# Kernel optimization log

Hardware: AMD Instinct MI355X
Metric: run time of the kernel (lower is better)

Reference implementation:

```python
import jax, jax.numpy as jnp
import numpy as np

DIM_IN, HID, N = 3, 512, 65536


def _xavier(key, shape):
    fan_in, fan_out = shape[1], shape[0]
    lim = np.sqrt(6.0 / (fan_in + fan_out))
    return jax.random.uniform(key, shape, jnp.float32, -lim, lim)


def setup_inputs() -> dict:
    key = jax.random.key(0)
    names_shapes = [
        ("W1", (HID, DIM_IN)), ("b1", (HID, 1)),
        ("Uz1", (HID, DIM_IN)), ("Wz1", (HID, HID)), ("bz1", (HID, 1)),
        ("Ug1", (HID, DIM_IN)), ("Wg1", (HID, HID)), ("bg1", (HID, 1)),
        ("Ur1", (HID, DIM_IN)), ("Wr1", (HID, HID)), ("br1", (HID, 1)),
        ("Uh1", (HID, DIM_IN)), ("Wh1", (HID, HID)), ("bh1", (HID, 1)),
        ("Uz2", (HID, DIM_IN)), ("Wz2", (HID, HID)), ("bz2", (HID, 1)),
        ("Ug2", (HID, DIM_IN)), ("Wg2", (HID, HID)), ("bg2", (HID, 1)),
        ("Ur2", (HID, DIM_IN)), ("Wr2", (HID, HID)), ("br2", (HID, 1)),
        ("Uh2", (HID, DIM_IN)), ("Wh2", (HID, HID)), ("bh2", (HID, 1)),
        ("W", (1, HID)), ("b", (1, 1)),
    ]
    keys = jax.random.split(key, len(names_shapes) + 1)
    inp = {"x": jax.random.normal(keys[0], (DIM_IN, N), jnp.float32)}
    for k, (nm, sh) in zip(keys[1:], names_shapes):
        inp[nm] = _xavier(k, sh)
    return inp


def reference(x, W1, b1, Uz1, Wz1, bz1, Ug1, Wg1, bg1, Ur1, Wr1, br1,
              Uh1, Wh1, bh1, Uz2, Wz2, bz2, Ug2, Wg2, bg2, Ur2, Wr2, br2,
              Uh2, Wh2, bh2, W, b):
    # x: (dim_in, N); all hidden states are (hidden_sz, N)
    S1 = jnp.tanh(W1 @ x + b1)
    Z1 = jnp.tanh(Uz1 @ x + Wz1 @ S1 + bz1)
    G1 = jnp.tanh(Ug1 @ x + Wg1 @ S1 + bg1)
    R1 = jnp.tanh(Ur1 @ x + Wr1 @ S1 + br1)
    H1 = jnp.tanh(Uh1 @ x + Wh1 @ (S1 * R1) + bh1)
    S2 = (1.0 - G1) * H1 + Z1 * S1
    Z2 = jnp.tanh(Uz2 @ x + Wz2 @ S2 + bz2)
    G2 = jnp.tanh(Ug2 @ x + Wg2 @ S2 + bg2)
    R2 = jnp.tanh(Ur2 @ x + Wr2 @ S2 + br2)
    H2 = jnp.tanh(Uh2 @ x + Wh2 @ (S2 * R2) + bh2)
    S3 = (1.0 - G2) * H2 + Z2 * S2
    return W @ S3 + b  # (1, N)
```

## Files before the change

### kernel.cpp

```cpp
#include <hip/hip_runtime.h>

typedef unsigned short u16;
typedef unsigned int   u32;
typedef short bf16x8 __attribute__((ext_vector_type(8)));
typedef float f32x4  __attribute__((ext_vector_type(4)));
typedef unsigned short u16x4 __attribute__((ext_vector_type(4)));
typedef unsigned int   u32x2 __attribute__((ext_vector_type(2)));

#define HID   512
#define NT    64
#define NCOL  65536
#define KTILES 17
#define BBUF  (KTILES * 4 * 512)
#define WMAT_ELEMS (KTILES * 32 * 512)

__device__ __forceinline__ float bf2f(u16 v) {
  union { u32 u; float f; } t; t.u = ((u32)v) << 16; return t.f;
}
__device__ __forceinline__ u16 f2bf(float f) {
  union { float f; u32 u; } t; t.f = f;
  u32 r = t.u + 0x7fffu + ((t.u >> 16) & 1u);
  return (u16)(r >> 16);
}
__device__ __forceinline__ float lo16(u32 v) { return bf2f((u16)(v & 0xffffu)); }
__device__ __forceinline__ float hi16(u32 v) { return bf2f((u16)(v >> 16)); }
__device__ __forceinline__ u32 pk2(float lo, float hi) {
  u32 r;
  asm("v_cvt_pk_bf16_f32 %0, %1, %2" : "=v"(r) : "v"(lo), "v"(hi));
  return r;
}
__device__ __forceinline__ float ldv(const void* p, int i, int isbf) {
  return isbf ? bf2f(((const u16*)p)[i]) : ((const float*)p)[i];
}
__device__ __forceinline__ float tanh_fast(float x) {
  float e = __builtin_amdgcn_exp2f(x * 2.8853900817779268f);
  return 1.0f - 2.0f * __builtin_amdgcn_rcpf(e + 1.0f);
}

__device__ __forceinline__ int boff(int c, int k) {
  return ((k >> 5) * 4 + (c >> 4)) * 512 + ((k >> 3) & 3) * 128 + (c & 15) * 8 + (k & 7);
}

__global__ void sniff_kernel(const u16* x, u32* flag) {
  if (threadIdx.x == 0 && blockIdx.x == 0) {
    int cnt = 0;
    for (int i = 0; i < 256; i++) {
      u32 e = (x[i] >> 7) & 0xFFu;
      if (e == 0u || (e >= 100u && e <= 140u)) cnt++;
    }
    *flag = (cnt >= 220) ? 1u : 0u;
  }
}

struct PrepArgs {
  const void* U[9]; const void* B[9];
  const void* Wout; const void* bout;
  float* dst; const u32* flag;
};

__global__ void prep_kernel(PrepArgs a) {
  int t = blockIdx.x * 256 + threadIdx.x;
  const int isbf = (int)*a.flag;
  if (t < 9 * 512) {
    int m = t >> 9, r = t & 511;
    float4 v;
    v.x = ldv(a.U[m], r * 3 + 0, isbf);
    v.y = ldv(a.U[m], r * 3 + 1, isbf);
    v.z = ldv(a.U[m], r * 3 + 2, isbf);
    v.w = ldv(a.B[m], r, isbf);
    ((float4*)a.dst)[t] = v;
  } else if (t < 9 * 512 + 512) {
    int r = t - 9 * 512;
    a.dst[9 * 2048 + r] = ldv(a.Wout, r, isbf);
    if (r == 0) a.dst[9 * 2048 + 512] = ldv(a.bout, 0, isbf);
  }
}

struct SwzArgs {
  const void* src[8];
  const void* usrc[8];
  const void* bsrc[8];
  u16* dst; const u32* flag;
};

__global__ void swizzle_kernel(SwzArgs a) {
  const int isbf = (int)*a.flag;
  int t = blockIdx.x * 256 + threadIdx.x;
  int m    = t / (KTILES * 32 * 64);
  int rem  = t - m * (KTILES * 32 * 64);
  int tile = rem >> 6;
  int lane = rem & 63;
  int kb = tile >> 5, rt = tile & 31;
  int row = rt * 16 + (lane & 15);
  int kk  = (lane >> 4) * 8;
  u16 tmp[8];
  if (kb < 16) {
    int k = kb * 32 + kk;
    if (isbf) {
      const u16* s = (const u16*)a.src[m] + row * 512 + k;
#pragma unroll
      for (int j = 0; j < 8; j++) tmp[j] = s[j];
    } else {
      const float* s = (const float*)a.src[m] + row * 512 + k;
#pragma unroll
      for (int j = 0; j < 8; j++) tmp[j] = f2bf(s[j]);
    }
  } else {
#pragma unroll
    for (int j = 0; j < 8; j++) {
      int kidx = kk + j;
      float v = (kidx < 3) ? ldv(a.usrc[m], row * 3 + kidx, isbf)
              : (kidx == 3) ? ldv(a.bsrc[m], row, isbf)
              : 0.0f;
      tmp[j] = f2bf(v);
    }
  }
  uint4* d = (uint4*)(a.dst + (size_t)m * WMAT_ELEMS + (size_t)tile * 512 + lane * 8);
  *d = *(const uint4*)tmp;
}

struct KArgs {
  const void* x;
  const u16* ws;
  const float4* ub;
  const u32* flag;
  void* out;
};

__device__ __forceinline__ void gemm64(f32x4 acc[4][4],
    const u16* __restrict__ wmat, const u16* ldsB, int rowslab, int lane)
{
  const u16* abase = wmat + (size_t)(rowslab * 4) * 512 + lane * 8;
  const u16* bbase = ldsB + lane * 8;
  bf16x8 a[3][4];
#pragma unroll
  for (int p = 0; p < 2; p++)
#pragma unroll
    for (int i = 0; i < 4; i++)
      a[p][i] = *(const bf16x8*)(abase + (size_t)p * 16384 + i * 512);
#pragma unroll
  for (int kb = 0; kb < KTILES; kb++) {
    if (kb + 2 < KTILES) {
#pragma unroll
      for (int i = 0; i < 4; i++)
        a[(kb + 2) % 3][i] = *(const bf16x8*)(abase + (size_t)(kb + 2) * 16384 + i * 512);
    }
    bf16x8 b[4];
#pragma unroll
    for (int ct = 0; ct < 4; ct++)
      b[ct] = *(const bf16x8*)(bbase + (kb * 4 + ct) * 512);
    __builtin_amdgcn_s_setprio(1);
#pragma unroll
    for (int rt = 0; rt < 4; rt++)
#pragma unroll
      for (int ct = 0; ct < 4; ct++)
        acc[rt][ct] = __builtin_amdgcn_mfma_f32_16x16x32_bf16(a[kb % 3][rt], b[ct], acc[rt][ct], 0, 0, 0);
    __builtin_amdgcn_s_setprio(0);
  }
}

__global__ __launch_bounds__(512, 2) void pdenet_kernel(KArgs ka) {
  __shared__ __align__(16) u16 ldsS[BBUF];
  __shared__ __align__(16) u16 ldsR[BBUF];
  __shared__ float xs[3 * NT];

  const int isbf = (int)*ka.flag;
  const int tid  = threadIdx.x;
  const int rowslab = tid >> 6;
  const int lane = tid & 63;
  const int l15  = lane & 15;
  const int quad = lane >> 4;
  const int c0   = blockIdx.x * NT;

  if (tid < 3 * NT)
    xs[tid] = ldv(ka.x, (tid >> 6) * NCOL + c0 + (tid & 63), isbf);
  __syncthreads();

  {
    int r = tid;
    float4 w = ka.ub[8 * 512 + r];
#pragma unroll 4
    for (int cc = 0; cc < NT; cc++) {
      int c = (cc + lane) & 63;
      float s = tanh_fast(w.x * xs[c] + w.y * xs[NT + c] + w.z * xs[2 * NT + c] + w.w);
      ldsS[boff(c, r)] = f2bf(s);
    }
  }

  {
#pragma unroll
    for (int rep = 0; rep < 4; rep++) {
      int e = tid + rep * 512;
      int c = e >> 5, j = e & 31;
      float v = (j == 0) ? xs[c] : (j == 1) ? xs[NT + c]
              : (j == 2) ? xs[2 * NT + c] : (j == 3) ? 1.0f : 0.0f;
      u16 bv = f2bf(v);
      int o = boff(c, 512 + j);
      ldsS[o] = bv;
      ldsR[o] = bv;
    }
  }
  __syncthreads();

  u32 zpk[4][4][2], opk[4][4][2];

#pragma unroll
  for (int layer = 0; layer < 2; layer++) {
    const int g0 = layer * 4;

    {
      f32x4 acc[4][4] = {};
      gemm64(acc, ka.ws + (size_t)(g0 + 0) * WMAT_ELEMS, ldsS, rowslab, lane);
#pragma unroll
      for (int rt = 0; rt < 4; rt++)
#pragma unroll
        for (int ct = 0; ct < 4; ct++) {
          zpk[rt][ct][0] = pk2(tanh_fast(acc[rt][ct][0]), tanh_fast(acc[rt][ct][1]));
          zpk[rt][ct][1] = pk2(tanh_fast(acc[rt][ct][2]), tanh_fast(acc[rt][ct][3]));
        }
    }
    {
      f32x4 acc[4][4] = {};
      gemm64(acc, ka.ws + (size_t)(g0 + 1) * WMAT_ELEMS, ldsS, rowslab, lane);
#pragma unroll
      for (int rt = 0; rt < 4; rt++)
#pragma unroll
        for (int ct = 0; ct < 4; ct++) {
          opk[rt][ct][0] = pk2(1.0f - tanh_fast(acc[rt][ct][0]),
                               1.0f - tanh_fast(acc[rt][ct][1]));
          opk[rt][ct][1] = pk2(1.0f - tanh_fast(acc[rt][ct][2]),
                               1.0f - tanh_fast(acc[rt][ct][3]));
        }
    }
    {
      f32x4 acc[4][4] = {};
      gemm64(acc, ka.ws + (size_t)(g0 + 2) * WMAT_ELEMS, ldsS, rowslab, lane);
#pragma unroll
      for (int rt = 0; rt < 4; rt++)
#pragma unroll
        for (int ct = 0; ct < 4; ct++) {
          int c  = ct * 16 + l15;
          int rb = rowslab * 64 + rt * 16 + quad * 4;
          int o  = boff(c, rb);
          u16x4 sv4 = *(const u16x4*)&ldsS[o];
          float sv0 = bf2f(sv4[0]), sv1 = bf2f(sv4[1]);
          float sv2 = bf2f(sv4[2]), sv3 = bf2f(sv4[3]);
          u32x2 sr;
          sr[0] = pk2(sv0 * tanh_fast(acc[rt][ct][0]), sv1 * tanh_fast(acc[rt][ct][1]));
          sr[1] = pk2(sv2 * tanh_fast(acc[rt][ct][2]), sv3 * tanh_fast(acc[rt][ct][3]));
          u32 zp0 = zpk[rt][ct][0], zp1 = zpk[rt][ct][1];
          zpk[rt][ct][0] = pk2(lo16(zp0) * sv0, hi16(zp0) * sv1);
          zpk[rt][ct][1] = pk2(lo16(zp1) * sv2, hi16(zp1) * sv3);
          *(u32x2*)&ldsR[o] = sr;
        }
    }
    __syncthreads();
    {
      f32x4 acc[4][4] = {};
      gemm64(acc, ka.ws + (size_t)(g0 + 3) * WMAT_ELEMS, ldsR, rowslab, lane);
#pragma unroll
      for (int rt = 0; rt < 4; rt++)
#pragma unroll
        for (int ct = 0; ct < 4; ct++) {
          int c  = ct * 16 + l15;
          int rb = rowslab * 64 + rt * 16 + quad * 4;
          u32 zp0 = zpk[rt][ct][0], zp1 = zpk[rt][ct][1];
          u32 op0 = opk[rt][ct][0], op1 = opk[rt][ct][1];
          u32x2 sn;
          sn[0] = pk2(lo16(op0) * tanh_fast(acc[rt][ct][0]) + lo16(zp0),
                      hi16(op0) * tanh_fast(acc[rt][ct][1]) + hi16(zp0));
          sn[1] = pk2(lo16(op1) * tanh_fast(acc[rt][ct][2]) + lo16(zp1),
                      hi16(op1) * tanh_fast(acc[rt][ct][3]) + hi16(zp1));
          *(u32x2*)&ldsS[boff(c, rb)] = sn;
        }
    }
    __syncthreads();
  }

  {
    int c   = tid >> 3;
    int seg = tid & 7;
    const float* wv = (const float*)(ka.ub + 9 * 512);
    const float4* w4 = (const float4*)(wv + seg * 64);
    float p = 0.0f;
#pragma unroll
    for (int j = 0; j < 16; j++) {
      u16x4 sv = *(const u16x4*)&ldsS[boff(c, seg * 64 + j * 4)];
      float4 w = w4[j];
      p += w.x * bf2f(sv[0]) + w.y * bf2f(sv[1]) + w.z * bf2f(sv[2]) + w.w * bf2f(sv[3]);
    }
    p += __shfl_xor(p, 1);
    p += __shfl_xor(p, 2);
    p += __shfl_xor(p, 4);
    if (seg == 0) {
      float res = p + wv[512];
      if (isbf) ((u16*)ka.out)[c0 + c] = f2bf(res);
      else      ((float*)ka.out)[c0 + c] = res;
    }
  }
}

extern "C" void kernel_launch(void* const* d_in, const int* in_sizes, int n_in,
                              void* d_out, int out_size, void* d_ws, size_t ws_size,
                              hipStream_t stream) {
  static const int widx[8] = {4, 7, 10, 13, 16, 19, 22, 25};
  static const int uidx[8] = {3, 6, 9, 12, 15, 18, 21, 24};
  static const int bidx[8] = {5, 8, 11, 14, 17, 20, 23, 26};

  u16*   ws16  = (u16*)d_ws;
  u32*   flagp = (u32*)((char*)d_ws + (size_t)8 * WMAT_ELEMS * 2);
  float* ubp   = (float*)((char*)d_ws + (size_t)8 * WMAT_ELEMS * 2 + 16);

  hipLaunchKernelGGL(sniff_kernel, dim3(1), dim3(64), 0, stream,
                     (const u16*)d_in[0], flagp);

  PrepArgs pa;
  for (int i = 0; i < 8; i++) { pa.U[i] = d_in[uidx[i]]; pa.B[i] = d_in[bidx[i]]; }
  pa.U[8] = d_in[1]; pa.B[8] = d_in[2];
  pa.Wout = d_in[27]; pa.bout = d_in[28];
  pa.dst = ubp; pa.flag = flagp;
  hipLaunchKernelGGL(prep_kernel, dim3(20), dim3(256), 0, stream, pa);

  SwzArgs sa;
  for (int i = 0; i < 8; i++) {
    sa.src[i]  = d_in[widx[i]];
    sa.usrc[i] = d_in[uidx[i]];
    sa.bsrc[i] = d_in[bidx[i]];
  }
  sa.dst  = ws16;
  sa.flag = flagp;
  hipLaunchKernelGGL(swizzle_kernel, dim3(1088), dim3(256), 0, stream, sa);

  KArgs ka;
  ka.x    = d_in[0];
  ka.ws   = ws16;
  ka.ub   = (const float4*)ubp;
  ka.flag = flagp;
  ka.out  = d_out;
  hipLaunchKernelGGL(pdenet_kernel, dim3(NCOL / NT), dim3(512), 0, stream, ka);
}
```

Measured before the change: 421.1 us.

## Overlap previous gate's tanh epilogue with next gate's MFMA loop

Adds a pipelined GEMM variant that, inside each K-tile iteration, applies tanh to one 16x16 accumulator tile of the previous gate (Z or G) and packs it to bf16 while the current gate's MFMAs issue. sched_group_barrier hints interleave the MFMAs with VALU work. The A-operand prefetch buffer also drops from three stages to two, which frees registers for the extra live accumulator set. The aim is to hide the transcendental epilogue behind matrix work, at the cost of keeping two 4x4 accumulator arrays live and possibly more register pressure or spills under launch_bounds(512,2).

```diff
diff --git a/kernel.cpp b/kernel.cpp
--- a/kernel.cpp
+++ b/kernel.cpp
@@ -132,18 +132,16 @@
 {
   const u16* abase = wmat + (size_t)(rowslab * 4) * 512 + lane * 8;
   const u16* bbase = ldsB + lane * 8;
-  bf16x8 a[3][4];
-#pragma unroll
-  for (int p = 0; p < 2; p++)
-#pragma unroll
-    for (int i = 0; i < 4; i++)
-      a[p][i] = *(const bf16x8*)(abase + (size_t)p * 16384 + i * 512);
+  bf16x8 a[2][4];
+#pragma unroll
+  for (int i = 0; i < 4; i++)
+    a[0][i] = *(const bf16x8*)(abase + i * 512);
 #pragma unroll
   for (int kb = 0; kb < KTILES; kb++) {
-    if (kb + 2 < KTILES) {
+    if (kb + 1 < KTILES) {
 #pragma unroll
       for (int i = 0; i < 4; i++)
-        a[(kb + 2) % 3][i] = *(const bf16x8*)(abase + (size_t)(kb + 2) * 16384 + i * 512);
+        a[(kb + 1) & 1][i] = *(const bf16x8*)(abase + (size_t)(kb + 1) * 16384 + i * 512);
     }
     bf16x8 b[4];
 #pragma unroll
@@ -154,8 +152,52 @@
     for (int rt = 0; rt < 4; rt++)
 #pragma unroll
       for (int ct = 0; ct < 4; ct++)
-        acc[rt][ct] = __builtin_amdgcn_mfma_f32_16x16x32_bf16(a[kb % 3][rt], b[ct], acc[rt][ct], 0, 0, 0);
+        acc[rt][ct] = __builtin_amdgcn_mfma_f32_16x16x32_bf16(a[kb & 1][rt], b[ct], acc[rt][ct], 0, 0, 0);
     __builtin_amdgcn_s_setprio(0);
+  }
+}
+
+template<int MODE>
+__device__ __forceinline__ void gemm64_pipe(f32x4 acc[4][4],
+    const u16* __restrict__ wmat, const u16* ldsB, int rowslab, int lane,
+    f32x4 accP[4][4], u32 dstP[4][4][2])
+{
+  const u16* abase = wmat + (size_t)(rowslab * 4) * 512 + lane * 8;
+  const u16* bbase = ldsB + lane * 8;
+  bf16x8 a[2][4];
+#pragma unroll
+  for (int i = 0; i < 4; i++)
+    a[0][i] = *(const bf16x8*)(abase + i * 512);
+#pragma unroll
+  for (int kb = 0; kb < KTILES; kb++) {
+    if (kb + 1 < KTILES) {
+#pragma unroll
+      for (int i = 0; i < 4; i++)
+        a[(kb + 1) & 1][i] = *(const bf16x8*)(abase + (size_t)(kb + 1) * 16384 + i * 512);
+    }
+    bf16x8 b[4];
+#pragma unroll
+    for (int ct = 0; ct < 4; ct++)
+      b[ct] = *(const bf16x8*)(bbase + (kb * 4 + ct) * 512);
+#pragma unroll
+    for (int rt = 0; rt < 4; rt++)
+#pragma unroll
+      for (int ct = 0; ct < 4; ct++)
+        acc[rt][ct] = __builtin_amdgcn_mfma_f32_16x16x32_bf16(a[kb & 1][rt], b[ct], acc[rt][ct], 0, 0, 0);
+    if (kb >= 1) {
+      const int i  = kb - 1;
+      const int rt = i >> 2;
+      const int ct = i & 3;
+      float t0 = tanh_fast(accP[rt][ct][0]);
+      float t1 = tanh_fast(accP[rt][ct][1]);
+      float t2 = tanh_fast(accP[rt][ct][2]);
+      float t3 = tanh_fast(accP[rt][ct][3]);
+      if (MODE) { t0 = 1.0f - t0; t1 = 1.0f - t1; t2 = 1.0f - t2; t3 = 1.0f - t3; }
+      dstP[rt][ct][0] = pk2(t0, t1);
+      dstP[rt][ct][1] = pk2(t2, t3);
+    }
+    __builtin_amdgcn_sched_group_barrier(0x008, 16, 0);
+    __builtin_amdgcn_sched_group_barrier(0x002, 30, 0);
   }
 }
 
@@ -208,33 +250,17 @@
   for (int layer = 0; layer < 2; layer++) {
     const int g0 = layer * 4;
 
+    f32x4 accZ[4][4] = {};
+    gemm64(accZ, ka.ws + (size_t)(g0 + 0) * WMAT_ELEMS, ldsS, rowslab, lane);
+
+    f32x4 accG[4][4] = {};
+    gemm64_pipe<0>(accG, ka.ws + (size_t)(g0 + 1) * WMAT_ELEMS, ldsS, rowslab,
+                   lane, accZ, zpk);
+
     {
       f32x4 acc[4][4] = {};
-      gemm64(acc, ka.ws + (size_t)(g0 + 0) * WMAT_ELEMS, ldsS, rowslab, lane);
-#pragma unroll
-      for (int rt = 0; rt < 4; rt++)
-#pragma unroll
-        for (int ct = 0; ct < 4; ct++) {
-          zpk[rt][ct][0] = pk2(tanh_fast(acc[rt][ct][0]), tanh_fast(acc[rt][ct][1]));
-          zpk[rt][ct][1] = pk2(tanh_fast(acc[rt][ct][2]), tanh_fast(acc[rt][ct][3]));
-        }
-    }
-    {
-      f32x4 acc[4][4] = {};
-      gemm64(acc, ka.ws + (size_t)(g0 + 1) * WMAT_ELEMS, ldsS, rowslab, lane);
-#pragma unroll
-      for (int rt = 0; rt < 4; rt++)
-#pragma unroll
-        for (int ct = 0; ct < 4; ct++) {
-          opk[rt][ct][0] = pk2(1.0f - tanh_fast(acc[rt][ct][0]),
-                               1.0f - tanh_fast(acc[rt][ct][1]));
-          opk[rt][ct][1] = pk2(1.0f - tanh_fast(acc[rt][ct][2]),
-                               1.0f - tanh_fast(acc[rt][ct][3]));
-        }
-    }
-    {
-      f32x4 acc[4][4] = {};
-      gemm64(acc, ka.ws + (size_t)(g0 + 2) * WMAT_ELEMS, ldsS, rowslab, lane);
+      gemm64_pipe<1>(acc, ka.ws + (size_t)(g0 + 2) * WMAT_ELEMS, ldsS, rowslab,
+                     lane, accG, opk);
 #pragma unroll
       for (int rt = 0; rt < 4; rt++)
 #pragma unroll
```

Measured after the change: 424.7 us. No clear change (+0.9%).

## Split row slabs across 16 waves with 1024-thread blocks

Applied to the files above, without the earlier changes.

Doubles the block to 1024 threads so each wave computes a 32-row slab (2 row tiles) instead of 64 rows, cutting per-wave accumulator and A-fragment registers and lowering the A prefetch depth from 2 tiles to 1. The S1 init, bias-row fill and final dot-product reduction are re-split across the larger thread count. The goal is more waves in flight to hide global weight-load latency, at the cost of each wave re-reading the shared B tiles from LDS for half as many MFMAs, a shallower prefetch, and more barrier participants.

```diff
diff --git a/kernel.cpp b/kernel.cpp
--- a/kernel.cpp
+++ b/kernel.cpp
@@ -127,23 +127,21 @@
   void* out;
 };
 
-__device__ __forceinline__ void gemm64(f32x4 acc[4][4],
-    const u16* __restrict__ wmat, const u16* ldsB, int rowslab, int lane)
+__device__ __forceinline__ void gemm64(f32x4 acc[2][4],
+    const u16* __restrict__ wmat, const u16* ldsB, int wave, int lane)
 {
-  const u16* abase = wmat + (size_t)(rowslab * 4) * 512 + lane * 8;
+  const u16* abase = wmat + (size_t)(wave * 2) * 512 + lane * 8;
   const u16* bbase = ldsB + lane * 8;
-  bf16x8 a[3][4];
-#pragma unroll
-  for (int p = 0; p < 2; p++)
-#pragma unroll
-    for (int i = 0; i < 4; i++)
-      a[p][i] = *(const bf16x8*)(abase + (size_t)p * 16384 + i * 512);
+  bf16x8 a[2][2];
+#pragma unroll
+  for (int i = 0; i < 2; i++)
+    a[0][i] = *(const bf16x8*)(abase + i * 512);
 #pragma unroll
   for (int kb = 0; kb < KTILES; kb++) {
-    if (kb + 2 < KTILES) {
-#pragma unroll
-      for (int i = 0; i < 4; i++)
-        a[(kb + 2) % 3][i] = *(const bf16x8*)(abase + (size_t)(kb + 2) * 16384 + i * 512);
+    if (kb + 1 < KTILES) {
+#pragma unroll
+      for (int i = 0; i < 2; i++)
+        a[(kb + 1) & 1][i] = *(const bf16x8*)(abase + (size_t)(kb + 1) * 16384 + i * 512);
     }
     bf16x8 b[4];
 #pragma unroll
@@ -151,22 +149,22 @@
       b[ct] = *(const bf16x8*)(bbase + (kb * 4 + ct) * 512);
     __builtin_amdgcn_s_setprio(1);
 #pragma unroll
-    for (int rt = 0; rt < 4; rt++)
+    for (int rt = 0; rt < 2; rt++)
 #pragma unroll
       for (int ct = 0; ct < 4; ct++)
-        acc[rt][ct] = __builtin_amdgcn_mfma_f32_16x16x32_bf16(a[kb % 3][rt], b[ct], acc[rt][ct], 0, 0, 0);
+        acc[rt][ct] = __builtin_amdgcn_mfma_f32_16x16x32_bf16(a[kb & 1][rt], b[ct], acc[rt][ct], 0, 0, 0);
     __builtin_amdgcn_s_setprio(0);
   }
 }
 
-__global__ __launch_bounds__(512, 2) void pdenet_kernel(KArgs ka) {
+__global__ __launch_bounds__(1024, 4) void pdenet_kernel(KArgs ka) {
   __shared__ __align__(16) u16 ldsS[BBUF];
   __shared__ __align__(16) u16 ldsR[BBUF];
   __shared__ float xs[3 * NT];
 
   const int isbf = (int)*ka.flag;
   const int tid  = threadIdx.x;
-  const int rowslab = tid >> 6;
+  const int wave = tid >> 6;
   const int lane = tid & 63;
   const int l15  = lane & 15;
   const int quad = lane >> 4;
@@ -177,11 +175,12 @@
   __syncthreads();
 
   {
-    int r = tid;
+    int r  = tid & 511;
+    int ch = tid >> 9;
     float4 w = ka.ub[8 * 512 + r];
 #pragma unroll 4
-    for (int cc = 0; cc < NT; cc++) {
-      int c = (cc + lane) & 63;
+    for (int cc = 0; cc < 32; cc++) {
+      int c = ch * 32 + ((cc + lane) & 31);
       float s = tanh_fast(w.x * xs[c] + w.y * xs[NT + c] + w.z * xs[2 * NT + c] + w.w);
       ldsS[boff(c, r)] = f2bf(s);
     }
@@ -189,8 +188,8 @@
 
   {
 #pragma unroll
-    for (int rep = 0; rep < 4; rep++) {
-      int e = tid + rep * 512;
+    for (int rep = 0; rep < 2; rep++) {
+      int e = tid + rep * 1024;
       int c = e >> 5, j = e & 31;
       float v = (j == 0) ? xs[c] : (j == 1) ? xs[NT + c]
               : (j == 2) ? xs[2 * NT + c] : (j == 3) ? 1.0f : 0.0f;
@@ -202,17 +201,17 @@
   }
   __syncthreads();
 
-  u32 zpk[4][4][2], opk[4][4][2];
+  u32 zpk[2][4][2], opk[2][4][2];
 
 #pragma unroll
   for (int layer = 0; layer < 2; layer++) {
     const int g0 = layer * 4;
 
     {
-      f32x4 acc[4][4] = {};
-      gemm64(acc, ka.ws + (size_t)(g0 + 0) * WMAT_ELEMS, ldsS, rowslab, lane);
-#pragma unroll
-      for (int rt = 0; rt < 4; rt++)
+      f32x4 acc[2][4] = {};
+      gemm64(acc, ka.ws + (size_t)(g0 + 0) * WMAT_ELEMS, ldsS, wave, lane);
+#pragma unroll
+      for (int rt = 0; rt < 2; rt++)
 #pragma unroll
         for (int ct = 0; ct < 4; ct++) {
           zpk[rt][ct][0] = pk2(tanh_fast(acc[rt][ct][0]), tanh_fast(acc[rt][ct][1]));
@@ -220,10 +219,10 @@
         }
     }
     {
-      f32x4 acc[4][4] = {};
-      gemm64(acc, ka.ws + (size_t)(g0 + 1) * WMAT_ELEMS, ldsS, rowslab, lane);
-#pragma unroll
-      for (int rt = 0; rt < 4; rt++)
+      f32x4 acc[2][4] = {};
+      gemm64(acc, ka.ws + (size_t)(g0 + 1) * WMAT_ELEMS, ldsS, wave, lane);
+#pragma unroll
+      for (int rt = 0; rt < 2; rt++)
 #pragma unroll
         for (int ct = 0; ct < 4; ct++) {
           opk[rt][ct][0] = pk2(1.0f - tanh_fast(acc[rt][ct][0]),
@@ -233,14 +232,14 @@
         }
     }
     {
-      f32x4 acc[4][4] = {};
-      gemm64(acc, ka.ws + (size_t)(g0 + 2) * WMAT_ELEMS, ldsS, rowslab, lane);
-#pragma unroll
-      for (int rt = 0; rt < 4; rt++)
+      f32x4 acc[2][4] = {};
+      gemm64(acc, ka.ws + (size_t)(g0 + 2) * WMAT_ELEMS, ldsS, wave, lane);
+#pragma unroll
+      for (int rt = 0; rt < 2; rt++)
 #pragma unroll
         for (int ct = 0; ct < 4; ct++) {
           int c  = ct * 16 + l15;
-          int rb = rowslab * 64 + rt * 16 + quad * 4;
+          int rb = wave * 32 + rt * 16 + quad * 4;
           int o  = boff(c, rb);
           u16x4 sv4 = *(const u16x4*)&ldsS[o];
           float sv0 = bf2f(sv4[0]), sv1 = bf2f(sv4[1]);
@@ -256,14 +255,14 @@
     }
     __syncthreads();
     {
-      f32x4 acc[4][4] = {};
-      gemm64(acc, ka.ws + (size_t)(g0 + 3) * WMAT_ELEMS, ldsR, rowslab, lane);
-#pragma unroll
-      for (int rt = 0; rt < 4; rt++)
+      f32x4 acc[2][4] = {};
+      gemm64(acc, ka.ws + (size_t)(g0 + 3) * WMAT_ELEMS, ldsR, wave, lane);
+#pragma unroll
+      for (int rt = 0; rt < 2; rt++)
 #pragma unroll
         for (int ct = 0; ct < 4; ct++) {
           int c  = ct * 16 + l15;
-          int rb = rowslab * 64 + rt * 16 + quad * 4;
+          int rb = wave * 32 + rt * 16 + quad * 4;
           u32 zp0 = zpk[rt][ct][0], zp1 = zpk[rt][ct][1];
           u32 op0 = opk[rt][ct][0], op1 = opk[rt][ct][1];
           u32x2 sn;
@@ -278,20 +277,21 @@
   }
 
   {
-    int c   = tid >> 3;
-    int seg = tid & 7;
+    int c   = tid >> 4;
+    int seg = tid & 15;
     const float* wv = (const float*)(ka.ub + 9 * 512);
-    const float4* w4 = (const float4*)(wv + seg * 64);
+    const float4* w4 = (const float4*)(wv + seg * 32);
     float p = 0.0f;
 #pragma unroll
-    for (int j = 0; j < 16; j++) {
-      u16x4 sv = *(const u16x4*)&ldsS[boff(c, seg * 64 + j * 4)];
+    for (int j = 0; j < 8; j++) {
+      u16x4 sv = *(const u16x4*)&ldsS[boff(c, seg * 32 + j * 4)];
       float4 w = w4[j];
       p += w.x * bf2f(sv[0]) + w.y * bf2f(sv[1]) + w.z * bf2f(sv[2]) + w.w * bf2f(sv[3]);
     }
     p += __shfl_xor(p, 1);
     p += __shfl_xor(p, 2);
     p += __shfl_xor(p, 4);
+    p += __shfl_xor(p, 8);
     if (seg == 0) {
       float res = p + wv[512];
       if (isbf) ((u16*)ka.out)[c0 + c] = f2bf(res);
@@ -337,5 +337,5 @@
   ka.ub   = (const float4*)ubp;
   ka.flag = flagp;
   ka.out  = d_out;
-  hipLaunchKernelGGL(pdenet_kernel, dim3(NCOL / NT), dim3(512), 0, stream, ka);
-}
+  hipLaunchKernelGGL(pdenet_kernel, dim3(NCOL / NT), dim3(1024), 0, stream, ka);
+}
```

Result: slower. 465.6 us (+10.6%).

## Spill 1-G gate to LDS and shrink A-prefetch to double buffer to cut VGPRs

Applied to the files above, without the earlier changes.

Moves the G-gate GEMM after the R-gate GEMM and stores (1-G) in the S buffer in LDS, after a barrier, instead of keeping it packed in registers. The last GEMM's epilogue then reads it back from LDS. The A-operand prefetch also goes from triple to double buffering. Both changes lower register pressure so the 512-thread, 2-block launch bound spills less, at the cost of extra LDS traffic and a shorter global-load prefetch distance.

```diff
diff --git a/kernel.cpp b/kernel.cpp
--- a/kernel.cpp
+++ b/kernel.cpp
@@ -132,18 +132,16 @@
 {
   const u16* abase = wmat + (size_t)(rowslab * 4) * 512 + lane * 8;
   const u16* bbase = ldsB + lane * 8;
-  bf16x8 a[3][4];
-#pragma unroll
-  for (int p = 0; p < 2; p++)
-#pragma unroll
-    for (int i = 0; i < 4; i++)
-      a[p][i] = *(const bf16x8*)(abase + (size_t)p * 16384 + i * 512);
+  bf16x8 a[2][4];
+#pragma unroll
+  for (int i = 0; i < 4; i++)
+    a[0][i] = *(const bf16x8*)(abase + i * 512);
 #pragma unroll
   for (int kb = 0; kb < KTILES; kb++) {
-    if (kb + 2 < KTILES) {
+    if (kb + 1 < KTILES) {
 #pragma unroll
       for (int i = 0; i < 4; i++)
-        a[(kb + 2) % 3][i] = *(const bf16x8*)(abase + (size_t)(kb + 2) * 16384 + i * 512);
+        a[(kb + 1) & 1][i] = *(const bf16x8*)(abase + (size_t)(kb + 1) * 16384 + i * 512);
     }
     bf16x8 b[4];
 #pragma unroll
@@ -154,7 +152,7 @@
     for (int rt = 0; rt < 4; rt++)
 #pragma unroll
       for (int ct = 0; ct < 4; ct++)
-        acc[rt][ct] = __builtin_amdgcn_mfma_f32_16x16x32_bf16(a[kb % 3][rt], b[ct], acc[rt][ct], 0, 0, 0);
+        acc[rt][ct] = __builtin_amdgcn_mfma_f32_16x16x32_bf16(a[kb & 1][rt], b[ct], acc[rt][ct], 0, 0, 0);
     __builtin_amdgcn_s_setprio(0);
   }
 }
@@ -202,7 +200,7 @@
   }
   __syncthreads();
 
-  u32 zpk[4][4][2], opk[4][4][2];
+  u32 zpk[4][4][2];
 
 #pragma unroll
   for (int layer = 0; layer < 2; layer++) {
@@ -217,19 +215,6 @@
         for (int ct = 0; ct < 4; ct++) {
           zpk[rt][ct][0] = pk2(tanh_fast(acc[rt][ct][0]), tanh_fast(acc[rt][ct][1]));
           zpk[rt][ct][1] = pk2(tanh_fast(acc[rt][ct][2]), tanh_fast(acc[rt][ct][3]));
-        }
-    }
-    {
-      f32x4 acc[4][4] = {};
-      gemm64(acc, ka.ws + (size_t)(g0 + 1) * WMAT_ELEMS, ldsS, rowslab, lane);
-#pragma unroll
-      for (int rt = 0; rt < 4; rt++)
-#pragma unroll
-        for (int ct = 0; ct < 4; ct++) {
-          opk[rt][ct][0] = pk2(1.0f - tanh_fast(acc[rt][ct][0]),
-                               1.0f - tanh_fast(acc[rt][ct][1]));
-          opk[rt][ct][1] = pk2(1.0f - tanh_fast(acc[rt][ct][2]),
-                               1.0f - tanh_fast(acc[rt][ct][3]));
         }
     }
     {
@@ -254,7 +239,22 @@
           *(u32x2*)&ldsR[o] = sr;
         }
     }
-    __syncthreads();
+    {
+      f32x4 acc[4][4] = {};
+      gemm64(acc, ka.ws + (size_t)(g0 + 1) * WMAT_ELEMS, ldsS, rowslab, lane);
+      __syncthreads();
+#pragma unroll
+      for (int rt = 0; rt < 4; rt++)
+#pragma unroll
+        for (int ct = 0; ct < 4; ct++) {
+          int c  = ct * 16 + l15;
+          int rb = rowslab * 64 + rt * 16 + quad * 4;
+          u32x2 og;
+          og[0] = pk2(1.0f - tanh_fast(acc[rt][ct][0]), 1.0f - tanh_fast(acc[rt][ct][1]));
+          og[1] = pk2(1.0f - tanh_fast(acc[rt][ct][2]), 1.0f - tanh_fast(acc[rt][ct][3]));
+          *(u32x2*)&ldsS[boff(c, rb)] = og;
+        }
+    }
     {
       f32x4 acc[4][4] = {};
       gemm64(acc, ka.ws + (size_t)(g0 + 3) * WMAT_ELEMS, ldsR, rowslab, lane);
@@ -264,14 +264,15 @@
         for (int ct = 0; ct < 4; ct++) {
           int c  = ct * 16 + l15;
           int rb = rowslab * 64 + rt * 16 + quad * 4;
+          int o  = boff(c, rb);
+          u16x4 og4 = *(const u16x4*)&ldsS[o];
           u32 zp0 = zpk[rt][ct][0], zp1 = zpk[rt][ct][1];
-          u32 op0 = opk[rt][ct][0], op1 = opk[rt][ct][1];
           u32x2 sn;
-          sn[0] = pk2(lo16(op0) * tanh_fast(acc[rt][ct][0]) + lo16(zp0),
-                      hi16(op0) * tanh_fast(acc[rt][ct][1]) + hi16(zp0));
-          sn[1] = pk2(lo16(op1) * tanh_fast(acc[rt][ct][2]) + lo16(zp1),
-                      hi16(op1) * tanh_fast(acc[rt][ct][3]) + hi16(zp1));
-          *(u32x2*)&ldsS[boff(c, rb)] = sn;
+          sn[0] = pk2(bf2f(og4[0]) * tanh_fast(acc[rt][ct][0]) + lo16(zp0),
+                      bf2f(og4[1]) * tanh_fast(acc[rt][ct][1]) + hi16(zp0));
+          sn[1] = pk2(bf2f(og4[2]) * tanh_fast(acc[rt][ct][2]) + lo16(zp1),
+                      bf2f(og4[3]) * tanh_fast(acc[rt][ct][3]) + hi16(zp1));
+          *(u32x2*)&ldsS[o] = sn;
         }
     }
     __syncthreads();
```

Result: no change. 420.5 us (-0.1%).
